# Optimization experiments

Measured on AMD Instinct MI355X. Metric: run time of the kernel, lower is better.

## Reference

```python
import jax, jax.numpy as jnp
import numpy as np

GRID_W, GRID_H = 4, 4          # num_splits = (4, 4) -> 16 experts
N = 524288                     # number of sample points
IN_DIM, HID, OUT = 2, 256, 3   # per-expert MLP: 2 -> 256 -> 3


def setup_inputs() -> dict:
    key = jax.random.key(0)
    k_s, k_w1, k_w2 = jax.random.split(key, 3)
    E = GRID_W * GRID_H
    samples = jax.random.uniform(k_s, (N, IN_DIM), dtype=jnp.float32)
    W1 = jax.random.normal(k_w1, (E, IN_DIM, HID), dtype=jnp.float32) * (1.0 / np.sqrt(IN_DIM))
    b1 = jnp.zeros((E, HID), dtype=jnp.float32)
    W2 = jax.random.normal(k_w2, (E, HID, OUT), dtype=jnp.float32) * (1.0 / np.sqrt(HID))
    b2 = jnp.zeros((E, OUT), dtype=jnp.float32)
    return {"samples": samples, "W1": W1, "b1": b1, "W2": W2, "b2": b2}


def _grid_inds(samples):
    # i, j = floor(samples[:, d] * n).clip(0, n-1); inds = j * w + i
    i = jnp.clip(jnp.floor(samples[:, 0] * GRID_W), 0, GRID_W - 1)
    j = jnp.clip(jnp.floor(samples[:, 1] * GRID_H), 0, GRID_H - 1)
    return (j * GRID_W + i).astype(jnp.int32)  # [N]


def reference(samples, W1, b1, W2, b2):
    inds = _grid_inds(samples)                     # [N] expert id per sample
    E = W1.shape[0]
    out = jnp.zeros((samples.shape[0], W2.shape[-1]), dtype=samples.dtype)
    # Dense dispatch: loop over the small fixed set of experts (16) and
    # select each sample's own expert output via the routing mask. Same
    # math as torch's features[inds == i] gather + scatter combine.
    for e in range(E):
        h = jax.nn.relu(samples @ W1[e] + b1[e])   # [N, HID]
        y = h @ W2[e] + b2[e]                      # [N, OUT]
        out = jnp.where((inds == e)[:, None], y, out)
    return out
```

## Files before the change

kernel.cpp:

```cpp
#include <hip/hip_runtime.h>

typedef _Float16 h2 __attribute__((ext_vector_type(2)));

#define GRID_W 4
#define GRID_H 4
#define NEXP   16
#define HID    256
#define TPB    1024
#define S      2
#define SAMP   (TPB * S)
#define NWAVE  (TPB / 64)
#define WPE    1536
#define GR     192
#define MAXENT 32

#define OFFB_B2   49152
#define OFFB_SLOT 49344
#define OFFB_INT  67264
#define LDS_BYTES 67856

union H8 { float4 f; h2 p[4]; };

template<int M>
__device__ __forceinline__ void mlp_fp16(const _Float16* __restrict__ W,
                                         const h2* px2, const h2* py2,
                                         float (*y)[3]) {
    const float4* W4 = (const float4*)W;
#pragma unroll 2
    for (int b = 0; b < 32; ++b) {
        H8 wa, wb, bb, u0, u1, u2;
        wa.f = W4[b];
        wb.f = W4[32 + b];
        bb.f = W4[64 + b];
        u0.f = W4[96 + b];
        u1.f = W4[128 + b];
        u2.f = W4[160 + b];
#pragma unroll
        for (int j = 0; j < 4; ++j) {
#pragma unroll
            for (int s = 0; s < M; ++s) {
                h2 h = __builtin_elementwise_fma(px2[s], wa.p[j],
                       __builtin_elementwise_fma(py2[s], wb.p[j], bb.p[j]));
                h2 z = (h2)(_Float16)0.0f;
                h = __builtin_elementwise_max(h, z);
#if __has_builtin(__builtin_amdgcn_fdot2)
                y[s][0] = __builtin_amdgcn_fdot2(h, u0.p[j], y[s][0], false);
                y[s][1] = __builtin_amdgcn_fdot2(h, u1.p[j], y[s][1], false);
                y[s][2] = __builtin_amdgcn_fdot2(h, u2.p[j], y[s][2], false);
#else
                y[s][0] += (float)h.x * (float)u0.p[j].x + (float)h.y * (float)u0.p[j].y;
                y[s][1] += (float)h.x * (float)u1.p[j].x + (float)h.y * (float)u1.p[j].y;
                y[s][2] += (float)h.x * (float)u2.p[j].x + (float)h.y * (float)u2.p[j].y;
#endif
            }
        }
    }
}

__global__ __launch_bounds__(TPB, 8) void fused_fp16_moe_kernel(
    const float2* __restrict__ samples,
    const float*  __restrict__ W1, const float* __restrict__ b1,
    const float*  __restrict__ W2, const float* __restrict__ b2,
    float* __restrict__ out, int N)
{
    extern __shared__ __align__(16) char smem[];
    _Float16* sWgt = (_Float16*)smem;
    float*    sB2  = (float*)(smem + OFFB_B2);
    int2*     sSlot= (int2*)(smem + OFFB_SLOT);
    int*      sI   = (int*)(smem + OFFB_INT);
    int* sHist = sI;
    int* sOff  = sI + 16;
    int* sES   = sI + 33;
    int* sEexp = sI + 50;
    int* sEbas = sI + 82;
    int* sEcnt = sI + 114;
    int* sC    = sI + 146;

    const int tid = threadIdx.x;

    if (tid < NEXP) sHist[tid] = 0;
    for (int t = tid; t < NEXP * 128; t += TPB) {
        int e = t >> 7, k2 = t & 127;
        const float2* ga = (const float2*)(W1 + e * 512);
        const float2* gb = (const float2*)(W1 + e * 512 + 256);
        const float2* gc = (const float2*)(b1 + e * 256);
        float2 A = ga[k2], B = gb[k2], Cc = gc[k2];
        h2* base = (h2*)(sWgt + e * WPE);
        h2 pa; pa.x = (_Float16)A.x;  pa.y = (_Float16)A.y;
        h2 pb; pb.x = (_Float16)B.x;  pb.y = (_Float16)B.y;
        h2 pc; pc.x = (_Float16)Cc.x; pc.y = (_Float16)Cc.y;
        base[k2]       = pa;
        base[128 + k2] = pb;
        base[256 + k2] = pc;
    }
    for (int t = tid; t < NEXP * 128; t += TPB) {
        int e = t >> 7, k2 = t & 127;
        const float2* g = (const float2*)(W2 + e * 768 + 6 * k2);
        float2 r0 = g[0], r1 = g[1], r2 = g[2];
        h2* base = (h2*)(sWgt + e * WPE);
        h2 p0; p0.x = (_Float16)r0.x; p0.y = (_Float16)r1.y;
        h2 p1; p1.x = (_Float16)r0.y; p1.y = (_Float16)r2.x;
        h2 p2; p2.x = (_Float16)r1.x; p2.y = (_Float16)r2.y;
        base[384 + k2] = p0;
        base[512 + k2] = p1;
        base[640 + k2] = p2;
    }
    if (tid < NEXP * 3) sB2[tid] = b2[tid];
    __syncthreads();

    const int base0 = blockIdx.x * SAMP;
    float px[S], py[S]; int eid[S], rank[S], gid[S]; bool act[S];
#pragma unroll
    for (int s = 0; s < S; ++s) {
        gid[s] = base0 + s * TPB + tid;
        act[s] = gid[s] < N;
        float2 p = act[s] ? samples[gid[s]] : make_float2(0.f, 0.f);
        px[s] = p.x; py[s] = p.y;
        int i = (int)(p.x * (float)GRID_W); i = i < 0 ? 0 : (i > GRID_W - 1 ? GRID_W - 1 : i);
        int j = (int)(p.y * (float)GRID_H); j = j < 0 ? 0 : (j > GRID_H - 1 ? GRID_H - 1 : j);
        eid[s] = j * GRID_W + i;
        rank[s] = act[s] ? atomicAdd(&sHist[eid[s]], 1) : 0;
    }
    __syncthreads();

    if (tid == 0) {
        int acc = 0, ec = 0;
        for (int e = 0; e < NEXP; ++e) {
            sOff[e] = acc; acc += sHist[e];
            sES[e] = ec;  ec  += (sHist[e] + GR - 1) / GR;
        }
        sOff[NEXP] = acc; sES[NEXP] = ec; *sC = ec;
    }
    __syncthreads();

#pragma unroll
    for (int s = 0; s < S; ++s) {
        if (act[s]) {
            union { h2 h; int i; } u;
            u.h.x = (_Float16)px[s]; u.h.y = (_Float16)py[s];
            int2 v; v.x = u.i; v.y = gid[s];
            sSlot[sOff[eid[s]] + rank[s]] = v;
        }
    }
    int C = *sC;
    if (tid < C) {
        int e = 0;
        while (tid >= sES[e + 1]) ++e;
        int j = tid - sES[e];
        sEexp[tid] = e;
        sEbas[tid] = sOff[e] + j * GR;
        sEcnt[tid] = min(GR, sHist[e] - j * GR);
    }
    __syncthreads();

    const int lane = tid & 63, wv = tid >> 6;
    for (int c = wv; c < C; c += NWAVE) {
        int e   = __builtin_amdgcn_readfirstlane(sEexp[c]);
        int bas = __builtin_amdgcn_readfirstlane(sEbas[c]);
        int cnt = __builtin_amdgcn_readfirstlane(sEcnt[c]);
        const _Float16* W = sWgt + e * WPE;
        float b20 = sB2[3 * e], b21 = sB2[3 * e + 1], b22 = sB2[3 * e + 2];
        int m = (cnt + 63) >> 6;

        h2 px2[3], py2[3]; int qg[3]; float yy[3][3];
#pragma unroll
        for (int s = 0; s < 3; ++s) {
            if (s < m) {
                int2 v = sSlot[bas + s * 64 + lane];
                union { int i; h2 h; } u; u.i = v.x;
                px2[s].x = u.h.x; px2[s].y = u.h.x;
                py2[s].x = u.h.y; py2[s].y = u.h.y;
                qg[s] = v.y;
                yy[s][0] = b20; yy[s][1] = b21; yy[s][2] = b22;
            }
        }

        if (m == 3)      mlp_fp16<3>(W, px2, py2, yy);
        else if (m == 2) mlp_fp16<2>(W, px2, py2, yy);
        else             mlp_fp16<1>(W, px2, py2, yy);

#pragma unroll
        for (int s = 0; s < 3; ++s) {
            if (s < m && s * 64 + lane < cnt) {
                int i3 = 3 * qg[s];
                out[i3 + 0] = yy[s][0];
                out[i3 + 1] = yy[s][1];
                out[i3 + 2] = yy[s][2];
            }
        }
    }
}

extern "C" void kernel_launch(void* const* d_in, const int* in_sizes, int n_in,
                              void* d_out, int out_size, void* d_ws, size_t ws_size,
                              hipStream_t stream) {
    const float* samples = (const float*)d_in[0];
    const float* W1      = (const float*)d_in[1];
    const float* b1      = (const float*)d_in[2];
    const float* W2      = (const float*)d_in[3];
    const float* b2      = (const float*)d_in[4];
    float* out = (float*)d_out;

    const int N = in_sizes[0] / 2;
    const int nblocks = (N + SAMP - 1) / SAMP;

    fused_fp16_moe_kernel<<<nblocks, TPB, LDS_BYTES, stream>>>(
        (const float2*)samples, W1, b1, W2, b2, out, N);
}
```

Before: 85.72 us.

## Pre-convert expert weights to fp16 in workspace and read them from global memory

```diff
diff --git a/kernel.cpp b/kernel.cpp
--- a/kernel.cpp
+++ b/kernel.cpp
@@ -14,19 +14,31 @@
 #define GR     192
 #define MAXENT 32
 
-#define OFFB_B2   49152
-#define OFFB_SLOT 49344
-#define OFFB_INT  67264
-#define LDS_BYTES 67856
+#define NSLOT  (SAMP + GR)
+#define OFFB_I (NSLOT * 8)
+#define LDS_BYTES (OFFB_I + 4 * (16 + 17 + 17 + 3 * MAXENT + 1))
+
+__global__ __launch_bounds__(256) void convert_kernel(
+    const float* __restrict__ W1, const float* __restrict__ b1,
+    const float* __restrict__ W2, _Float16* __restrict__ wsW) {
+    int t = blockIdx.x * 256 + threadIdx.x;
+    int e = t >> 8, k = t & 255;
+    _Float16* dst = wsW + e * WPE;
+    dst[k]        = (_Float16)W1[e * 512 + k];
+    dst[256 + k]  = (_Float16)W1[e * 512 + 256 + k];
+    dst[512 + k]  = (_Float16)b1[e * 256 + k];
+    dst[768 + k]  = (_Float16)W2[e * 768 + 3 * k];
+    dst[1024 + k] = (_Float16)W2[e * 768 + 3 * k + 1];
+    dst[1280 + k] = (_Float16)W2[e * 768 + 3 * k + 2];
+}
 
 union H8 { float4 f; h2 p[4]; };
 
 template<int M>
-__device__ __forceinline__ void mlp_fp16(const _Float16* __restrict__ W,
+__device__ __forceinline__ void mlp_pass(const float4* __restrict__ W4,
                                          const h2* px2, const h2* py2,
                                          float (*y)[3]) {
-    const float4* W4 = (const float4*)W;
-#pragma unroll 2
+#pragma unroll 4
     for (int b = 0; b < 32; ++b) {
         H8 wa, wb, bb, u0, u1, u2;
         wa.f = W4[b];
@@ -57,55 +69,25 @@
     }
 }
 
-__global__ __launch_bounds__(TPB, 8) void fused_fp16_moe_kernel(
+__global__ __launch_bounds__(TPB) void fused_smem_moe_kernel(
     const float2* __restrict__ samples,
-    const float*  __restrict__ W1, const float* __restrict__ b1,
-    const float*  __restrict__ W2, const float* __restrict__ b2,
+    const _Float16* __restrict__ wsW,
+    const float* __restrict__ b2,
     float* __restrict__ out, int N)
 {
     extern __shared__ __align__(16) char smem[];
-    _Float16* sWgt = (_Float16*)smem;
-    float*    sB2  = (float*)(smem + OFFB_B2);
-    int2*     sSlot= (int2*)(smem + OFFB_SLOT);
-    int*      sI   = (int*)(smem + OFFB_INT);
+    int2* sSlot = (int2*)smem;
+    int*  sI    = (int*)(smem + OFFB_I);
     int* sHist = sI;
     int* sOff  = sI + 16;
     int* sES   = sI + 33;
     int* sEexp = sI + 50;
-    int* sEbas = sI + 82;
-    int* sEcnt = sI + 114;
-    int* sC    = sI + 146;
+    int* sEbas = sI + 50 + MAXENT;
+    int* sEcnt = sI + 50 + 2 * MAXENT;
+    int* sC    = sI + 50 + 3 * MAXENT;
 
     const int tid = threadIdx.x;
-
     if (tid < NEXP) sHist[tid] = 0;
-    for (int t = tid; t < NEXP * 128; t += TPB) {
-        int e = t >> 7, k2 = t & 127;
-        const float2* ga = (const float2*)(W1 + e * 512);
-        const float2* gb = (const float2*)(W1 + e * 512 + 256);
-        const float2* gc = (const float2*)(b1 + e * 256);
-        float2 A = ga[k2], B = gb[k2], Cc = gc[k2];
-        h2* base = (h2*)(sWgt + e * WPE);
-        h2 pa; pa.x = (_Float16)A.x;  pa.y = (_Float16)A.y;
-        h2 pb; pb.x = (_Float16)B.x;  pb.y = (_Float16)B.y;
-        h2 pc; pc.x = (_Float16)Cc.x; pc.y = (_Float16)Cc.y;
-        base[k2]       = pa;
-        base[128 + k2] = pb;
-        base[256 + k2] = pc;
-    }
-    for (int t = tid; t < NEXP * 128; t += TPB) {
-        int e = t >> 7, k2 = t & 127;
-        const float2* g = (const float2*)(W2 + e * 768 + 6 * k2);
-        float2 r0 = g[0], r1 = g[1], r2 = g[2];
-        h2* base = (h2*)(sWgt + e * WPE);
-        h2 p0; p0.x = (_Float16)r0.x; p0.y = (_Float16)r1.y;
-        h2 p1; p1.x = (_Float16)r0.y; p1.y = (_Float16)r2.x;
-        h2 p2; p2.x = (_Float16)r1.x; p2.y = (_Float16)r2.y;
-        base[384 + k2] = p0;
-        base[512 + k2] = p1;
-        base[640 + k2] = p2;
-    }
-    if (tid < NEXP * 3) sB2[tid] = b2[tid];
     __syncthreads();
 
     const int base0 = blockIdx.x * SAMP;
@@ -158,8 +140,8 @@
         int e   = __builtin_amdgcn_readfirstlane(sEexp[c]);
         int bas = __builtin_amdgcn_readfirstlane(sEbas[c]);
         int cnt = __builtin_amdgcn_readfirstlane(sEcnt[c]);
-        const _Float16* W = sWgt + e * WPE;
-        float b20 = sB2[3 * e], b21 = sB2[3 * e + 1], b22 = sB2[3 * e + 2];
+        const float4* W4 = (const float4*)(wsW + e * WPE);
+        float b20 = b2[3 * e], b21 = b2[3 * e + 1], b22 = b2[3 * e + 2];
         int m = (cnt + 63) >> 6;
 
         h2 px2[3], py2[3]; int qg[3]; float yy[3][3];
@@ -175,9 +157,9 @@
             }
         }
 
-        if (m == 3)      mlp_fp16<3>(W, px2, py2, yy);
-        else if (m == 2) mlp_fp16<2>(W, px2, py2, yy);
-        else             mlp_fp16<1>(W, px2, py2, yy);
+        if (m == 3)      mlp_pass<3>(W4, px2, py2, yy);
+        else if (m == 2) mlp_pass<2>(W4, px2, py2, yy);
+        else             mlp_pass<1>(W4, px2, py2, yy);
 
 #pragma unroll
         for (int s = 0; s < 3; ++s) {
@@ -202,8 +184,11 @@
     float* out = (float*)d_out;
 
     const int N = in_sizes[0] / 2;
+    _Float16* wsW = (_Float16*)d_ws;
+
+    convert_kernel<<<NEXP, 256, 0, stream>>>(W1, b1, W2, wsW);
+
     const int nblocks = (N + SAMP - 1) / SAMP;
-
-    fused_fp16_moe_kernel<<<nblocks, TPB, LDS_BYTES, stream>>>(
-        (const float2*)samples, W1, b1, W2, b2, out, N);
+    fused_smem_moe_kernel<<<nblocks, TPB, LDS_BYTES, stream>>>(
+        (const float2*)samples, wsW, b2, out, N);
 }
```

After: 85.04 us. About the same (-0.8%).
